# Performance work log

Measured on AMD Instinct MI355X. Metric: run time of the kernel, lower is better.

Reference implementation:

```python
import jax, jax.numpy as jnp
import numpy as np

N_HEAD = 12
CTX = 2048
FUT = 16
EPS = 1e-5


def _layer_norm(x, w, b):
    m = x.mean(-1, keepdims=True)
    v = ((x - m) ** 2).mean(-1, keepdims=True)
    return (x - m) / jnp.sqrt(v + EPS) * w + b


def setup_inputs() -> dict:
    key = jax.random.key(0)
    ks = jax.random.split(key, 10)
    C = 768
    hs = C // N_HEAD
    B, T = 1, 2048
    std = 0.02
    inp = {
        "x": jax.random.normal(ks[0], (B, T, C), jnp.float32),
        "ln1_w": jnp.ones((C,), jnp.float32),
        "ln1_b": jnp.zeros((C,), jnp.float32),
        "attn_w": jax.random.normal(ks[1], (C, 3 * C), jnp.float32) * std,
        "attn_b": jnp.zeros((3 * C,), jnp.float32),
        "fk_w": jax.random.normal(ks[2], (N_HEAD, hs, CTX - 1), jnp.float32) * std,
        "fk_b": jnp.zeros((N_HEAD, 1, CTX - 1), jnp.float32),
        "fv_w": jax.random.normal(ks[3], (N_HEAD, CTX - 1, hs), jnp.float32) * std,
        "fv_b": jnp.zeros((N_HEAD, 1, hs), jnp.float32),
        "proj_w": jax.random.normal(ks[4], (C, C), jnp.float32) * std,
        "proj_b": jnp.zeros((C,), jnp.float32),
        "ln2_w": jnp.ones((C,), jnp.float32),
        "ln2_b": jnp.zeros((C,), jnp.float32),
        "ff_w1": jax.random.normal(ks[5], (C, 4 * C), jnp.float32) * std,
        "ff_b1": jnp.zeros((4 * C,), jnp.float32),
        "ff_w2": jax.random.normal(ks[6], (4 * C, C), jnp.float32) * std,
        "ff_b2": jnp.zeros((C,), jnp.float32),
    }
    return inp


def _block(x, ln1_w, ln1_b, attn_w, attn_b, fk_w, fk_b, fv_w, fv_b,
           proj_w, proj_b, ln2_w, ln2_b, ff_w1, ff_b1, ff_w2, ff_b2):
    B, T, C = x.shape
    hs = C // N_HEAD
    T_wf = min(T + FUT, CTX)          # static
    F1 = T_wf - 1
    scale = hs ** (-0.5)

    h = _layer_norm(x, ln1_w, ln1_b)
    qkv = h @ attn_w + attn_b
    q, k, v = jnp.split(qkv, 3, axis=-1)
    q = q.reshape(B, T, N_HEAD, hs).transpose(0, 2, 1, 3)  # [B,H,T,hs]
    k = k.reshape(B, T, N_HEAD, hs).transpose(0, 2, 1, 3)
    v = v.reshape(B, T, N_HEAD, hs).transpose(0, 2, 1, 3)

    attn = jnp.einsum('bhqd,bhkd->bhqk', q, k) * scale      # [B,H,T,T]

    causal = jnp.tril(jnp.ones((T, T), bool))
    causal_attn = jnp.where(causal, attn, 0.0)
    pad = min(FUT, CTX - T)
    if pad > 0:
        causal_attn = jnp.pad(causal_attn, ((0, 0), (0, 0), (0, 0), (0, pad)))

    # future scores via per-head dynamic linear on q
    fut_bad = (jnp.tril(jnp.ones((T, F1)), -1) + jnp.triu(jnp.ones((T, F1)), FUT)) != 0
    fattn = (jnp.einsum('bhtd,hdf->bhtf', q, fk_w[:, :, :F1]) + fk_b[:, :, :F1]) * scale
    fattn = jnp.where(fut_bad, 0.0, fattn)
    fattn = jnp.pad(fattn, ((0, 0), (0, 0), (0, 0), (1, 0)))  # [B,H,T,T_wf]

    full = causal_attn + fattn
    full_ok = jnp.tril(jnp.ones((T, T_wf), bool), FUT)
    full = jnp.where(full_ok, full, -jnp.inf)
    sm = jax.nn.softmax(full, axis=-1)

    sc = jnp.where(causal, sm[..., :T], 0.0)
    sf = jnp.where(fut_bad, 0.0, sm[..., 1:T_wf])

    causal_x = jnp.einsum('bhqk,bhkd->bhqd', sc, v)
    future_x = jnp.einsum('bhtf,hfd->bhtd', sf, fv_w[:, :F1, :]) + fv_b

    new_x = (causal_x + future_x).transpose(0, 2, 1, 3).reshape(B, T, C)
    new_x = new_x @ proj_w + proj_b

    x = x + new_x
    h2 = _layer_norm(x, ln2_w, ln2_b)
    ff = jax.nn.gelu(h2 @ ff_w1 + ff_b1, approximate=False) @ ff_w2 + ff_b2
    return x + ff


def reference(x, ln1_w, ln1_b, attn_w, attn_b, fk_w, fk_b, fv_w, fv_b,
              proj_w, proj_b, ln2_w, ln2_b, ff_w1, ff_b1, ff_w2, ff_b2):
    return _block(x, ln1_w, ln1_b, attn_w, attn_b, fk_w, fk_b, fv_w, fv_b,
                  proj_w, proj_b, ln2_w, ln2_b, ff_w1, ff_b1, ff_w2, ff_b2)
```

## Files before the change

kernel.cpp:

```cpp
#include <hip/hip_runtime.h>
#include <math.h>
#include <stdint.h>
#include <stddef.h>

typedef __bf16 bf16_t;
typedef __bf16 bf16x8 __attribute__((ext_vector_type(8)));
typedef float f32x4 __attribute__((ext_vector_type(4)));

#define DEV __device__ __forceinline__


DEV void gload_lds16(const void* g, void* l) {
  __builtin_amdgcn_global_load_lds((__attribute__((address_space(1))) void*)g,
                                   (__attribute__((address_space(3))) void*)l,
                                   16, 0, 0);
}

template <bool MAXOP>
DEV float blockReduce256(float v, float* sm) {
  const int lane = threadIdx.x & 63, wid = threadIdx.x >> 6;
#pragma unroll
  for (int o = 32; o > 0; o >>= 1) {
    float ov = __shfl_down(v, o);
    v = MAXOP ? fmaxf(v, ov) : (v + ov);
  }
  if (lane == 0) sm[wid] = v;
  __syncthreads();
  float r = MAXOP ? fmaxf(fmaxf(sm[0], sm[1]), fmaxf(sm[2], sm[3]))
                  : (sm[0] + sm[1] + sm[2] + sm[3]);
  __syncthreads();
  return r;
}

__global__ __launch_bounds__(256) void ln_kernel(const float* __restrict__ x,
                                                 const float* __restrict__ w,
                                                 const float* __restrict__ b,
                                                 bf16_t* __restrict__ out) {
  __shared__ float red[4];
  const int t = blockIdx.x, tid = threadIdx.x;
  const float* row = x + (size_t)t * 768;
  float v[3];
  float s = 0.f;
#pragma unroll
  for (int i = 0; i < 3; ++i) {
    v[i] = row[tid + i * 256];
    s += v[i];
  }
  s = blockReduce256<false>(s, red);
  const float mean = s * (1.f / 768.f);
  float s2 = 0.f;
#pragma unroll
  for (int i = 0; i < 3; ++i) {
    float d = v[i] - mean;
    s2 += d * d;
  }
  s2 = blockReduce256<false>(s2, red);
  const float rstd = rsqrtf(s2 * (1.f / 768.f) + 1e-5f);
#pragma unroll
  for (int i = 0; i < 3; ++i) {
    int c = tid + i * 256;
    out[(size_t)t * 768 + c] = (bf16_t)((v[i] - mean) * rstd * w[c] + b[c]);
  }
}

__global__ __launch_bounds__(256) void reduce_ln_kernel(
    const float* __restrict__ P, int KS, const float* __restrict__ x,
    const float* __restrict__ pb, float* __restrict__ x2,
    bf16_t* __restrict__ h2, const float* __restrict__ w,
    const float* __restrict__ b) {
  __shared__ float red[4];
  const int t = blockIdx.x, tid = threadIdx.x;
  float v[3];
  float s = 0.f;
#pragma unroll
  for (int i = 0; i < 3; ++i) {
    const int c = tid + i * 256;
    const size_t idx = (size_t)t * 768 + c;
    float a = x[idx] + pb[c];
    for (int ss = 0; ss < KS; ++ss) a += P[(size_t)ss * 2048 * 768 + idx];
    v[i] = a;
    x2[idx] = a;
    s += a;
  }
  s = blockReduce256<false>(s, red);
  const float mean = s * (1.f / 768.f);
  float s2 = 0.f;
#pragma unroll
  for (int i = 0; i < 3; ++i) {
    float d = v[i] - mean;
    s2 += d * d;
  }
  s2 = blockReduce256<false>(s2, red);
  const float rstd = rsqrtf(s2 * (1.f / 768.f) + 1e-5f);
#pragma unroll
  for (int i = 0; i < 3; ++i) {
    int c = tid + i * 256;
    h2[(size_t)t * 768 + c] = (bf16_t)((v[i] - mean) * rstd * w[c] + b[c]);
  }
}

__global__ __launch_bounds__(256) void reduce_out_kernel(
    const float* __restrict__ P, int KS, const float* __restrict__ x2,
    const float* __restrict__ bb, float* __restrict__ out) {
  const int t = blockIdx.x, tid = threadIdx.x;
#pragma unroll
  for (int i = 0; i < 3; ++i) {
    const int c = tid + i * 256;
    const size_t idx = (size_t)t * 768 + c;
    float a = x2[idx] + bb[c];
    for (int ss = 0; ss < KS; ++ss) a += P[(size_t)ss * 2048 * 768 + idx];
    out[idx] = a;
  }
}

template <typename TIN>
__global__ void transpose_to_b(const TIN* __restrict__ in, long long sInZ, int ldin,
                               bf16_t* __restrict__ out, long long sOutZ, int ldout,
                               int R, int Cc) {
  __shared__ float tile[32][33];
  in += (long long)blockIdx.z * sInZ;
  out += (long long)blockIdx.z * sOutZ;
  const int c0 = blockIdx.x * 32, r0 = blockIdx.y * 32;
  const int tx = threadIdx.x, ty = threadIdx.y;
#pragma unroll
  for (int i = 0; i < 4; ++i) {
    int r = r0 + ty + i * 8, c = c0 + tx;
    if (r < R && c < Cc) tile[ty + i * 8][tx] = (float)in[(size_t)r * ldin + c];
  }
  __syncthreads();
#pragma unroll
  for (int i = 0; i < 4; ++i) {
    int orow = c0 + ty + i * 8, oc = r0 + tx;
    if (orow < Cc && oc < R) out[(size_t)orow * ldout + oc] = (bf16_t)tile[tx][ty + i * 8];
  }
}

template <int WM, int WN, int EPIL, bool OBF16>
__global__ __launch_bounds__(256) void gemm_bt_kernel(
    const bf16_t* __restrict__ A, long long sAz, int lda,
    const bf16_t* __restrict__ Bt, long long sBz, int ldb,
    void* __restrict__ Cv, long long sCz, int ldc,
    const float* __restrict__ bias,
    const float* __restrict__ resid, long long sRz,
    float alpha, int M, int N, int K) {
  constexpr int BM = WM * 64, BN = WN * 64;
  const int tid = threadIdx.x;
  const int lane = tid & 63, wid = tid >> 6;
  const int wr = wid / WN, wc = wid % WN;
  const int m0 = blockIdx.y * BM, n0 = blockIdx.x * BN;
  A += (long long)blockIdx.z * sAz;
  Bt += (long long)blockIdx.z * sBz;

  __shared__ alignas(16) bf16_t sA[2][BM * 32];
  __shared__ alignas(16) bf16_t sB[2][BN * 32];

  f32x4 acc[4][4] = {};

  auto stage = [&](int buf, int k0) {
#pragma unroll
    for (int it = 0; it < (BM * 4) / 256; ++it) {
      int c = it * 256 + tid;
      gload_lds16(A + (size_t)(m0 + (c >> 2)) * (size_t)lda + k0 + (c & 3) * 8,
                  &sA[buf][c * 8]);
    }
#pragma unroll
    for (int it = 0; it < (BN * 4) / 256; ++it) {
      int c = it * 256 + tid;
      gload_lds16(Bt + (size_t)(n0 + (c >> 2)) * (size_t)ldb + k0 + (c & 3) * 8,
                  &sB[buf][c * 8]);
    }
  };

  const int nk = K >> 5;
  stage(0, 0);
  __syncthreads();
  for (int ki = 0; ki < nk; ++ki) {
    if (ki + 1 < nk) stage((ki + 1) & 1, (ki + 1) << 5);
    const bf16_t* cA = sA[ki & 1];
    const bf16_t* cB = sB[ki & 1];
    bf16x8 af[4], bfr[4];
#pragma unroll
    for (int i = 0; i < 4; ++i) {
      af[i] = *(const bf16x8*)&cA[(wr * 64 + i * 16 + (lane & 15)) * 32 + 8 * (lane >> 4)];
      bfr[i] = *(const bf16x8*)&cB[(wc * 64 + i * 16 + (lane & 15)) * 32 + 8 * (lane >> 4)];
    }
#pragma unroll
    for (int mi = 0; mi < 4; ++mi)
#pragma unroll
      for (int ni = 0; ni < 4; ++ni)
        acc[mi][ni] = __builtin_amdgcn_mfma_f32_16x16x32_bf16(af[mi], bfr[ni], acc[mi][ni], 0, 0, 0);
    __syncthreads();
  }

  float* Cf = (float*)Cv;
  bf16_t* Cb = (bf16_t*)Cv;
  const long long zc = (long long)blockIdx.z * sCz;
#pragma unroll
  for (int mi = 0; mi < 4; ++mi) {
    const int rbase = m0 + wr * 64 + mi * 16 + ((lane >> 4) * 4);
#pragma unroll
    for (int ni = 0; ni < 4; ++ni) {
      const int col = n0 + wc * 64 + ni * 16 + (lane & 15);
      const float bv = bias ? bias[col] : 0.f;
#pragma unroll
      for (int r = 0; r < 4; ++r) {
        const int row = rbase + r;
        float v = acc[mi][ni][r] * alpha + bv;
        if (EPIL == 1) v = 0.5f * v * (1.f + erff(v * 0.70710678118654752f));
        if (resid) v += resid[(long long)blockIdx.z * sRz + (size_t)row * ldc + col];
        const size_t idx = (size_t)(zc + (long long)row * ldc + col);
        if (OBF16)
          Cb[idx] = (bf16_t)v;
        else
          Cf[idx] = v;
      }
    }
  }
}

#define FLASH_TPW 8
#define FLASH_NSLOT 5
#define FLASH_BANDPART 4
__global__ __launch_bounds__(256) void flash_kernel(
    const bf16_t* __restrict__ qkv, const bf16_t* __restrict__ vT,
    const bf16_t* __restrict__ fkT, const bf16_t* __restrict__ fvT,
    const float* __restrict__ fk_b, float* __restrict__ Ouc,
    float* __restrict__ lsum) {
  const int qt = 31 - (int)blockIdx.x, h = blockIdx.y, part = blockIdx.z;
  const int ntiles = qt + 1;
  const int q0 = qt << 6;
  const int tid = threadIdx.x, lane = tid & 63, w = tid >> 6;
  __shared__ alignas(16) bf16_t sK[2][64 * 64];
  __shared__ alignas(16) bf16_t sV[2][64 * 64];
  __shared__ alignas(16) bf16_t sP[4][16 * 128];

  const int l15 = lane & 15, l4 = lane >> 4;
  const int rloc = w * 16 + (l4 << 2);
  const int rowC0 = q0 + rloc;
  bf16_t* sPw = sP[w];

  if (part != FLASH_BANDPART) {
    const int kt0 = part * FLASH_TPW;
    if (kt0 >= ntiles) return;
  }

  const int qrow = q0 + w * 16 + l15;
  bf16x8 aq[2];
#pragma unroll
  for (int kk = 0; kk < 2; ++kk)
    aq[kk] = *(const bf16x8*)&qkv[(size_t)qrow * 2304 + h * 64 + 8 * l4 + 32 * kk];

  f32x4 o[4] = {};
  float lacc[4] = {0.f, 0.f, 0.f, 0.f};

  if (part == FLASH_BANDPART) {
    const int t0 = q0;
    bf16_t* sKb = &sK[0][0];
    bf16_t* sVb = &sV[0][0];
#pragma unroll
    for (int it = 0; it < 3; ++it) {
      const int c = it * 256 + tid;
      if (c < 640) {
        const int row = c >> 3, slot = c & 7;
        const int ss = slot ^ (row & 7);
        const int srow = min(t0 + row, 2046);
        gload_lds16(fkT + ((size_t)h * 2047 + srow) * 64 + ss * 8, &sKb[c * 8]);
      }
    }
#pragma unroll
    for (int it = 0; it < 4; ++it) {
      const int c = it * 256 + tid;
      const int row = c >> 4, slot = c & 15;
      const int ss = slot ^ (row & 7);
      gload_lds16(fvT + ((size_t)h * 64 + row) * 2048 + t0 + ss * 8, &sVb[c * 8]);
    }
    __syncthreads();

    f32x4 s[6] = {};
#pragma unroll
    for (int kk = 0; kk < 2; ++kk)
#pragma unroll
      for (int ni = 0; ni < 5; ++ni) {
        const int row = ni * 16 + l15;
        const int slot = l4 + 4 * kk;
        bf16x8 bfk = *(const bf16x8*)&sKb[row * 64 + ((slot ^ (row & 7)) * 8)];
        s[ni] = __builtin_amdgcn_mfma_f32_16x16x32_bf16(aq[kk], bfk, s[ni], 0, 0, 0);
      }
    float fkb_v[5];
#pragma unroll
    for (int ni = 0; ni < 5; ++ni)
      fkb_v[ni] = fk_b[h * 2047 + min(t0 + ni * 16 + l15, 2046)];

#pragma unroll
    for (int ni = 0; ni < 6; ++ni) {
      const int c = ni * 16 + l15;
      const int colb = c * 2;
#pragma unroll
      for (int r = 0; r < 4; ++r) {
        const int j = c - (rloc + r);
        const bool ok = (ni < 5) && (j >= 0) && (j < 16) && (t0 + c < 2047);
        const float pv = ok ? __expf((s[ni][r] + fkb_v[ni < 5 ? ni : 0]) * 0.125f) : 0.f;
        lacc[r] += pv;
        const int pr = (l4 << 2) + r;
        *(bf16_t*)((char*)sPw + ((pr * 256 + colb) ^ ((pr & 7) << 4))) = (bf16_t)pv;
      }
    }

#pragma unroll
    for (int kk = 0; kk < 3; ++kk) {
      const int slot = l4 + 4 * kk;
      bf16x8 ap = *(const bf16x8*)((char*)sPw + (l15 * 256 + ((slot ^ (l15 & 7)) * 16)));
#pragma unroll
      for (int ni = 0; ni < 4; ++ni) {
        const int vrow = ni * 16 + l15;
        bf16x8 bv = *(const bf16x8*)&sVb[vrow * 128 + ((slot ^ (vrow & 7)) * 8)];
        o[ni] = __builtin_amdgcn_mfma_f32_16x16x32_bf16(ap, bv, o[ni], 0, 0, 0);
      }
    }
  } else {
    const int kt0 = part * FLASH_TPW;
    const int kt1 = min(kt0 + FLASH_TPW, ntiles);

    auto stage = [&](int buf, int kt) {
      const int t0 = kt << 6;
#pragma unroll
      for (int it = 0; it < 2; ++it) {
        const int c = it * 256 + tid;
        const int row = c >> 3, slot = c & 7;
        const int ss = slot ^ (row & 7);
        gload_lds16(qkv + (size_t)(t0 + row) * 2304 + 768 + h * 64 + ss * 8,
                    &sK[buf][c * 8]);
        gload_lds16(vT + ((size_t)h * 64 + row) * 2048 + t0 + ss * 8,
                    &sV[buf][c * 8]);
      }
    };

    stage(0, kt0);
    __syncthreads();

    for (int kt = kt0; kt < kt1; ++kt) {
      const int buf = (kt - kt0) & 1;
      if (kt + 1 < kt1) stage(buf ^ 1, kt + 1);
      const int t0 = kt << 6;

      f32x4 s[4] = {};
#pragma unroll
      for (int kk = 0; kk < 2; ++kk)
#pragma unroll
        for (int ni = 0; ni < 4; ++ni) {
          const int row = ni * 16 + l15;
          const int slot = l4 + 4 * kk;
          bf16x8 bfk = *(const bf16x8*)&sK[buf][row * 64 + ((slot ^ (row & 7)) * 8)];
          s[ni] = __builtin_amdgcn_mfma_f32_16x16x32_bf16(aq[kk], bfk, s[ni], 0, 0, 0);
        }

      const bool full = (t0 + 63 <= q0);
#pragma unroll
      for (int ni = 0; ni < 4; ++ni) {
        const int col = t0 + ni * 16 + l15;
        const int colb = (ni * 16 + l15) * 2;
#pragma unroll
        for (int r = 0; r < 4; ++r) {
          const bool ok = full || (col <= rowC0 + r);
          const float pv = ok ? __expf(s[ni][r] * 0.125f) : 0.f;
          lacc[r] += pv;
          const int pr = (l4 << 2) + r;
          *(bf16_t*)((char*)sPw + ((pr * 256 + colb) ^ ((pr & 7) << 4))) = (bf16_t)pv;
        }
      }

#pragma unroll
      for (int kk = 0; kk < 2; ++kk) {
        const int slot = l4 + 4 * kk;
        bf16x8 ap = *(const bf16x8*)((char*)sPw + (l15 * 256 + ((slot ^ (l15 & 7)) * 16)));
#pragma unroll
        for (int ni = 0; ni < 4; ++ni) {
          const int vrow = ni * 16 + l15;
          bf16x8 bv = *(const bf16x8*)&sV[buf][vrow * 64 + ((slot ^ (vrow & 7)) * 8)];
          o[ni] = __builtin_amdgcn_mfma_f32_16x16x32_bf16(ap, bv, o[ni], 0, 0, 0);
        }
      }
      __syncthreads();
    }
  }

  float* Oh = Ouc + (((size_t)h * 32 + qt) * FLASH_NSLOT + part) * 4096;
#pragma unroll
  for (int ni = 0; ni < 4; ++ni) {
    const int col = ni * 16 + l15;
#pragma unroll
    for (int r = 0; r < 4; ++r) Oh[(size_t)(rloc + r) * 64 + col] = o[ni][r];
  }
#pragma unroll
  for (int off = 1; off < 16; off <<= 1)
#pragma unroll
    for (int r = 0; r < 4; ++r) lacc[r] += __shfl_xor(lacc[r], off);
  if (l15 == 0) {
#pragma unroll
    for (int r = 0; r < 4; ++r)
      lsum[((size_t)h * 2048 + rowC0 + r) * FLASH_NSLOT + part] = lacc[r];
  }
}

__global__ __launch_bounds__(256) void combine_kernel(
    const float* __restrict__ Ouc, const float* __restrict__ lsum,
    const float* __restrict__ fv_b, bf16_t* __restrict__ attn_o) {
  const int t = blockIdx.x * 4 + (threadIdx.x >> 6);
  const int h = blockIdx.y, lane = threadIdx.x & 63;
  const int qt = t >> 6;
  const int nparts = (qt + FLASH_TPW) / FLASH_TPW;
  const float* Ob = Ouc + ((size_t)h * 32 + qt) * FLASH_NSLOT * 4096 +
                    (t & 63) * 64 + lane;
  const float* lb = lsum + ((size_t)h * 2048 + t) * FLASH_NSLOT;
  float l_run = lb[FLASH_BANDPART];
  float O_run = Ob[(size_t)FLASH_BANDPART * 4096];
  for (int p = 0; p < nparts; ++p) {
    l_run += lb[p];
    O_run += Ob[(size_t)p * 4096];
  }
  const float val = O_run / l_run + fv_b[h * 64 + lane];
  attn_o[(size_t)t * 768 + h * 64 + lane] = (bf16_t)val;
}


extern "C" void kernel_launch(void* const* d_in, const int* in_sizes, int n_in,
                              void* d_out, int out_size, void* d_ws, size_t ws_size,
                              hipStream_t stream) {
  (void)in_sizes; (void)n_in; (void)out_size;
  const float* x      = (const float*)d_in[0];
  const float* ln1_w  = (const float*)d_in[1];
  const float* ln1_b  = (const float*)d_in[2];
  const float* attn_w = (const float*)d_in[3];
  const float* attn_b = (const float*)d_in[4];
  const float* fk_w   = (const float*)d_in[5];
  const float* fk_b   = (const float*)d_in[6];
  const float* fv_w   = (const float*)d_in[7];
  const float* fv_b   = (const float*)d_in[8];
  const float* proj_w = (const float*)d_in[9];
  const float* proj_b = (const float*)d_in[10];
  const float* ln2_w  = (const float*)d_in[11];
  const float* ln2_b  = (const float*)d_in[12];
  const float* ff_w1  = (const float*)d_in[13];
  const float* ff_b1  = (const float*)d_in[14];
  const float* ff_w2  = (const float*)d_in[15];
  const float* ff_b2  = (const float*)d_in[16];
  float* out = (float*)d_out;

  char* wsp = (char*)d_ws;
  size_t off = 0;
  auto alloc = [&](size_t bytes) -> void* {
    void* r = wsp + off;
    off += (bytes + 255) & ~(size_t)255;
    return r;
  };

  bf16_t* hbuf    = (bf16_t*)alloc((size_t)2048 * 768 * 2);
  bf16_t* attn_wT = (bf16_t*)alloc((size_t)2304 * 768 * 2);
  bf16_t* proj_wT = (bf16_t*)alloc((size_t)768 * 768 * 2);
  bf16_t* ff_w1T  = (bf16_t*)alloc((size_t)3072 * 768 * 2);
  bf16_t* ff_w2T  = (bf16_t*)alloc((size_t)768 * 3072 * 2);
  bf16_t* fkT     = (bf16_t*)alloc((size_t)12 * 2047 * 64 * 2);
  bf16_t* fvT     = (bf16_t*)alloc(((size_t)12 * 64 * 2048 + 512) * 2);
  bf16_t* qkv     = (bf16_t*)alloc((size_t)2048 * 2304 * 2);
  bf16_t* vT      = (bf16_t*)alloc((size_t)12 * 64 * 2048 * 2);
  bf16_t* attn_o  = (bf16_t*)alloc((size_t)2048 * 768 * 2);
  float*  x2      = (float*)alloc((size_t)2048 * 768 * 4);
  bf16_t* h2      = (bf16_t*)alloc((size_t)2048 * 768 * 2);
  bf16_t* gbuf    = (bf16_t*)alloc((size_t)2048 * 3072 * 2);
  float*  Ouc     = (float*)alloc((size_t)12 * 32 * FLASH_NSLOT * 4096 * 4);
  float*  lsb     = (float*)alloc((size_t)12 * 2048 * FLASH_NSLOT * 4);

  const size_t slice = (size_t)2048 * 768 * 4;
  long long remain = ((long long)ws_size - (long long)off) / (long long)slice;
  int KS2 = 6;
  while (KS2 > 1 && ((3072 / KS2) % 32 != 0 || (3072 % KS2) != 0 || KS2 > remain)) --KS2;
  int KS1 = 4;
  while (KS1 > 1 && ((768 / KS1) % 32 != 0 || (768 % KS1) != 0 || KS1 > remain)) --KS1;
  int KSmax = KS1 > KS2 ? KS1 : KS2;
  float* Ppart = (float*)alloc((size_t)KSmax * slice);

  ln_kernel<<<2048, 256, 0, stream>>>(x, ln1_w, ln1_b, hbuf);

  transpose_to_b<float><<<dim3(72, 24, 1), dim3(32, 8), 0, stream>>>(
      attn_w, 0, 2304, attn_wT, 0, 768, 768, 2304);
  transpose_to_b<float><<<dim3(24, 24, 1), dim3(32, 8), 0, stream>>>(
      proj_w, 0, 768, proj_wT, 0, 768, 768, 768);
  transpose_to_b<float><<<dim3(96, 24, 1), dim3(32, 8), 0, stream>>>(
      ff_w1, 0, 3072, ff_w1T, 0, 768, 768, 3072);
  transpose_to_b<float><<<dim3(24, 96, 1), dim3(32, 8), 0, stream>>>(
      ff_w2, 0, 768, ff_w2T, 0, 3072, 3072, 768);
  transpose_to_b<float><<<dim3(64, 2, 12), dim3(32, 8), 0, stream>>>(
      fk_w, 64LL * 2047, 2047, fkT, 2047LL * 64, 64, 64, 2047);
  transpose_to_b<float><<<dim3(2, 64, 12), dim3(32, 8), 0, stream>>>(
      fv_w, 2047LL * 64, 64, fvT, 64LL * 2048, 2048, 2047, 64);

  gemm_bt_kernel<2, 2, 0, true><<<dim3(18, 16, 1), 256, 0, stream>>>(
      hbuf, 0, 768, attn_wT, 0, 768, qkv, 0, 2304, attn_b, nullptr, 0, 1.f,
      2048, 2304, 768);

  transpose_to_b<bf16_t><<<dim3(2, 64, 12), dim3(32, 8), 0, stream>>>(
      qkv + 1536, 64, 2304, vT, 64LL * 2048, 2048, 2048, 64);

  flash_kernel<<<dim3(32, 12, FLASH_NSLOT), 256, 0, stream>>>(
      qkv, vT, fkT, fvT, fk_b, Ouc, lsb);

  combine_kernel<<<dim3(512, 12), 256, 0, stream>>>(Ouc, lsb, fv_b, attn_o);

  {
    const int KC = 768 / KS1;
    gemm_bt_kernel<2, 2, 0, false><<<dim3(6, 16, KS1), 256, 0, stream>>>(
        attn_o, KC, 768, proj_wT, KC, 768, Ppart, 2048LL * 768, 768, nullptr,
        nullptr, 0, 1.f, 2048, 768, KC);
  }
  reduce_ln_kernel<<<2048, 256, 0, stream>>>(Ppart, KS1, x, proj_b, x2, h2,
                                             ln2_w, ln2_b);

  gemm_bt_kernel<2, 2, 1, true><<<dim3(24, 16, 1), 256, 0, stream>>>(
      h2, 0, 768, ff_w1T, 0, 768, gbuf, 0, 3072, ff_b1, nullptr, 0, 1.f, 2048,
      3072, 768);

  {
    const int KC = 3072 / KS2;
    gemm_bt_kernel<2, 2, 0, false><<<dim3(6, 16, KS2), 256, 0, stream>>>(
        gbuf, KC, 3072, ff_w2T, KC, 3072, Ppart, 2048LL * 768, 768, nullptr,
        nullptr, 0, 1.f, 2048, 768, KC);
  }
  reduce_out_kernel<<<2048, 256, 0, stream>>>(Ppart, KS2, x2, ff_b2, out);
}
```

Baseline: 175.4 us.

## Replace 4-wave GEMM with single-wave 64x64 tile GEMM without block barriers

Each GEMM now uses one wavefront per 64x64 output tile instead of four waves sharing a 128x128 tile. Because only one wave touches its LDS buffers, the __syncthreads calls are dropped and explicit vmcnt waits are used to overlap the next tile's global-to-LDS load with the current MFMAs. Launch grids grow about fourfold, and the FFN2 split-K factor drops from 6 to 4. The cost is less reuse of operands per LDS load, which means more global traffic, and the correctness of the double buffer now depends on the vmcnt ordering.

Result: slower. 191.9 us (+9.4%).

```diff
diff --git a/kernel.cpp b/kernel.cpp
--- a/kernel.cpp
+++ b/kernel.cpp
@@ -135,37 +135,34 @@
   }
 }
 
-template <int WM, int WN, int EPIL, bool OBF16>
-__global__ __launch_bounds__(256) void gemm_bt_kernel(
+template <int EPIL, bool OBF16>
+__global__ __launch_bounds__(64) void gemm_w64_kernel(
     const bf16_t* __restrict__ A, long long sAz, int lda,
     const bf16_t* __restrict__ Bt, long long sBz, int ldb,
     void* __restrict__ Cv, long long sCz, int ldc,
     const float* __restrict__ bias,
     const float* __restrict__ resid, long long sRz,
     float alpha, int M, int N, int K) {
-  constexpr int BM = WM * 64, BN = WN * 64;
-  const int tid = threadIdx.x;
-  const int lane = tid & 63, wid = tid >> 6;
-  const int wr = wid / WN, wc = wid % WN;
-  const int m0 = blockIdx.y * BM, n0 = blockIdx.x * BN;
+  const int lane = threadIdx.x;
+  const int m0 = blockIdx.y * 64, n0 = blockIdx.x * 64;
   A += (long long)blockIdx.z * sAz;
   Bt += (long long)blockIdx.z * sBz;
 
-  __shared__ alignas(16) bf16_t sA[2][BM * 32];
-  __shared__ alignas(16) bf16_t sB[2][BN * 32];
+  __shared__ alignas(16) bf16_t sA[2][64 * 32];
+  __shared__ alignas(16) bf16_t sB[2][64 * 32];
 
   f32x4 acc[4][4] = {};
 
   auto stage = [&](int buf, int k0) {
 #pragma unroll
-    for (int it = 0; it < (BM * 4) / 256; ++it) {
-      int c = it * 256 + tid;
+    for (int it = 0; it < 4; ++it) {
+      int c = it * 64 + lane;
       gload_lds16(A + (size_t)(m0 + (c >> 2)) * (size_t)lda + k0 + (c & 3) * 8,
                   &sA[buf][c * 8]);
     }
 #pragma unroll
-    for (int it = 0; it < (BN * 4) / 256; ++it) {
-      int c = it * 256 + tid;
+    for (int it = 0; it < 4; ++it) {
+      int c = it * 64 + lane;
       gload_lds16(Bt + (size_t)(n0 + (c >> 2)) * (size_t)ldb + k0 + (c & 3) * 8,
                   &sB[buf][c * 8]);
     }
@@ -173,23 +170,28 @@
 
   const int nk = K >> 5;
   stage(0, 0);
-  __syncthreads();
   for (int ki = 0; ki < nk; ++ki) {
-    if (ki + 1 < nk) stage((ki + 1) & 1, (ki + 1) << 5);
-    const bf16_t* cA = sA[ki & 1];
-    const bf16_t* cB = sB[ki & 1];
+    const int buf = ki & 1;
+    if (ki + 1 < nk) {
+      stage(buf ^ 1, (ki + 1) << 5);
+      asm volatile("s_waitcnt vmcnt(8)" ::: "memory");
+    } else {
+      asm volatile("s_waitcnt vmcnt(0)" ::: "memory");
+    }
+    __builtin_amdgcn_sched_barrier(0);
+    const bf16_t* cA = sA[buf];
+    const bf16_t* cB = sB[buf];
     bf16x8 af[4], bfr[4];
 #pragma unroll
     for (int i = 0; i < 4; ++i) {
-      af[i] = *(const bf16x8*)&cA[(wr * 64 + i * 16 + (lane & 15)) * 32 + 8 * (lane >> 4)];
-      bfr[i] = *(const bf16x8*)&cB[(wc * 64 + i * 16 + (lane & 15)) * 32 + 8 * (lane >> 4)];
+      af[i] = *(const bf16x8*)&cA[(i * 16 + (lane & 15)) * 32 + 8 * (lane >> 4)];
+      bfr[i] = *(const bf16x8*)&cB[(i * 16 + (lane & 15)) * 32 + 8 * (lane >> 4)];
     }
 #pragma unroll
     for (int mi = 0; mi < 4; ++mi)
 #pragma unroll
       for (int ni = 0; ni < 4; ++ni)
         acc[mi][ni] = __builtin_amdgcn_mfma_f32_16x16x32_bf16(af[mi], bfr[ni], acc[mi][ni], 0, 0, 0);
-    __syncthreads();
   }
 
   float* Cf = (float*)Cv;
@@ -197,10 +199,10 @@
   const long long zc = (long long)blockIdx.z * sCz;
 #pragma unroll
   for (int mi = 0; mi < 4; ++mi) {
-    const int rbase = m0 + wr * 64 + mi * 16 + ((lane >> 4) * 4);
+    const int rbase = m0 + mi * 16 + ((lane >> 4) * 4);
 #pragma unroll
     for (int ni = 0; ni < 4; ++ni) {
-      const int col = n0 + wc * 64 + ni * 16 + (lane & 15);
+      const int col = n0 + ni * 16 + (lane & 15);
       const float bv = bias ? bias[col] : 0.f;
 #pragma unroll
       for (int r = 0; r < 4; ++r) {
@@ -472,7 +474,7 @@
 
   const size_t slice = (size_t)2048 * 768 * 4;
   long long remain = ((long long)ws_size - (long long)off) / (long long)slice;
-  int KS2 = 6;
+  int KS2 = 4;
   while (KS2 > 1 && ((3072 / KS2) % 32 != 0 || (3072 % KS2) != 0 || KS2 > remain)) --KS2;
   int KS1 = 4;
   while (KS1 > 1 && ((768 / KS1) % 32 != 0 || (768 % KS1) != 0 || KS1 > remain)) --KS1;
@@ -494,7 +496,7 @@
   transpose_to_b<float><<<dim3(2, 64, 12), dim3(32, 8), 0, stream>>>(
       fv_w, 2047LL * 64, 64, fvT, 64LL * 2048, 2048, 2047, 64);
 
-  gemm_bt_kernel<2, 2, 0, true><<<dim3(18, 16, 1), 256, 0, stream>>>(
+  gemm_w64_kernel<0, true><<<dim3(36, 32, 1), 64, 0, stream>>>(
       hbuf, 0, 768, attn_wT, 0, 768, qkv, 0, 2304, attn_b, nullptr, 0, 1.f,
       2048, 2304, 768);
 
@@ -508,20 +510,20 @@
 
   {
     const int KC = 768 / KS1;
-    gemm_bt_kernel<2, 2, 0, false><<<dim3(6, 16, KS1), 256, 0, stream>>>(
+    gemm_w64_kernel<0, false><<<dim3(12, 32, KS1), 64, 0, stream>>>(
         attn_o, KC, 768, proj_wT, KC, 768, Ppart, 2048LL * 768, 768, nullptr,
         nullptr, 0, 1.f, 2048, 768, KC);
   }
   reduce_ln_kernel<<<2048, 256, 0, stream>>>(Ppart, KS1, x, proj_b, x2, h2,
                                              ln2_w, ln2_b);
 
-  gemm_bt_kernel<2, 2, 1, true><<<dim3(24, 16, 1), 256, 0, stream>>>(
+  gemm_w64_kernel<1, true><<<dim3(48, 32, 1), 64, 0, stream>>>(
       h2, 0, 768, ff_w1T, 0, 768, gbuf, 0, 3072, ff_b1, nullptr, 0, 1.f, 2048,
       3072, 768);
 
   {
     const int KC = 3072 / KS2;
-    gemm_bt_kernel<2, 2, 0, false><<<dim3(6, 16, KS2), 256, 0, stream>>>(
+    gemm_w64_kernel<0, false><<<dim3(12, 32, KS2), 64, 0, stream>>>(
         gbuf, KC, 3072, ff_w2T, KC, 3072, Ppart, 2048LL * 768, 768, nullptr,
         nullptr, 0, 1.f, 2048, 768, KC);
   }
```
